# Kernel optimization log

Measured on AMD Instinct MI355X. Metric: run time of the kernel, lower is better.

Reference implementation:

```python
import jax, jax.numpy as jnp
import numpy as np

POOL = 3            # pool_size for this detection level
CENTER_TOP_NUM = 100
CENTER_THRES = 0.1
INST_THRES = 0.4


def _pool2d(x, op, k):
    """Stride-1 SAME pooling on NCHW, matching torch pad=(k-1)//2.
    avg matches torch avg_pool2d default count_include_pad=True (divide by k*k)."""
    if op == 'max':
        return jax.lax.reduce_window(x, -jnp.inf, jax.lax.max,
                                     (1, 1, k, k), (1, 1, 1, 1), 'SAME')
    s = jax.lax.reduce_window(x, 0.0, jax.lax.add,
                              (1, 1, k, k), (1, 1, 1, 1), 'SAME')
    return s / (k * k)


def setup_inputs() -> dict:
    key = jax.random.key(0)
    k1, k2, k3 = jax.random.split(key, 3)
    return {
        'thing_map':    jax.random.normal(k1, (1, 80, 128, 256), jnp.float32),
        'kernel_space': jax.random.normal(k2, (1, 256, 128, 256), jnp.float32),
        'embeddings':   jax.random.normal(k3, (1, 256, 256, 512), jnp.float32),
    }


def reference(thing_map, kernel_space, embeddings):
    B, C, H, W = thing_map.shape
    # --- peak detection (CenterNet-style) ---
    centers = jax.nn.sigmoid(thing_map)
    centers = (centers + _pool2d(centers, 'avg', POOL)) * 0.5
    fmap_max = _pool2d(centers, 'max', 3)
    peak_mask = (fmap_max == centers).astype(centers.dtype)
    centers = centers * peak_mask
    # --- topk over (class, h, w) ---
    K = min(H * W, CENTER_TOP_NUM // 2)  # 50
    flat = centers.reshape(B, C * H * W)
    scores, idx = jax.lax.top_k(flat, K)          # [B, K], sorted descending
    cats = idx // (H * W)                          # [B, K] class ids
    spatial = idx % (H * W)                        # [B, K] spatial index
    # masked_select(score > thres) replaced by a static-shape validity mask
    valid = (scores > CENTER_THRES).astype(scores.dtype)
    # --- sample kernels at peak locations ---
    D = kernel_space.shape[1]
    kflat = kernel_space.reshape(B, D, H * W)      # batch dims (h w)
    kernels = jnp.take_along_axis(kflat, spatial[:, None, :], axis=2)  # [B, D, K]
    kernels = kernels.transpose(0, 2, 1)           # [B, K, D]
    # --- maskifier: dynamic conv of kernels over embeddings, then sigmoid ---
    thing_masks = jax.nn.sigmoid(
        jnp.einsum('bkd,bdhw->bkhw', kernels, embeddings))  # [B, K, He, We]
    # --- mask-based score rescoring ---
    binm = (thing_masks > INST_THRES).astype(thing_masks.dtype)
    score_factor = (thing_masks * binm).sum((-2, -1))
    score_factor = score_factor / jnp.maximum(binm.sum((-2, -1)), 1e-8)
    scores = scores * score_factor * valid
    return thing_masks, scores, cats
```

## Files before the change

### kernel.cpp

```cpp
#include <hip/hip_runtime.h>
#include <hip/hip_bf16.h>
#include <math.h>


constexpr int C   = 80;
constexpr int H   = 128;
constexpr int W   = 256;
constexpr int HW  = H * W;
constexpr int CHW = C * HW;
constexpr int D   = 256;
constexpr int NPIX = 256 * 512;
constexpr int K   = 50;
constexpr int KP  = 52;
constexpr int NBINS = 4096;
constexpr int NREP  = 16;
constexpr int MAXCAND = 8192;
constexpr int SEL_CAP = 4096;
constexpr int MASK_ELEMS = K * NPIX;

constexpr int NBLK  = C * 128;
constexpr int SLOTS = 64;
constexpr int CAP   = NBLK * SLOTS;

constexpr int OFF_PKVAL  = 0;
constexpr int OFF_PKIDX  = CAP;
constexpr int OFF_PKCNT  = 2 * CAP;
constexpr int OFF_HIST   = OFF_PKCNT + NBLK;
constexpr int OFF_CUTBIN = OFF_HIST + NREP * NBINS;
constexpr int OFF_CCOUNT = OFF_CUTBIN + 1;
constexpr int OFF_FNUM   = OFF_CCOUNT + 1;
constexpr int OFF_FDEN   = OFF_FNUM + K;
constexpr int OFF_CVAL   = OFF_FDEN + K;
constexpr int OFF_CIDX   = OFF_CVAL + MAXCAND;
constexpr int OFF_TSCORE = OFF_CIDX + MAXCAND;
constexpr int OFF_TSPAT  = OFF_TSCORE + K;
constexpr int OFF_TCAT   = OFF_TSPAT + K;
constexpr int OFF_A      = (OFF_TCAT + K + 3) & ~3;
constexpr int ZERO_WORDS = NREP * NBINS + 2 + 2 * K;

#define REP13(X) X(0) X(1) X(2) X(3) X(4) X(5) X(6) X(7) X(8) X(9) X(10) X(11) X(12)

__device__ __forceinline__ float sigmoidf(float x) {
    return 1.0f / (1.0f + expf(-x));
}

__device__ __forceinline__ int value_bin(float v) {
    int b = (int)(v * (float)NBINS);
    return b > NBINS - 1 ? NBINS - 1 : b;
}

constexpr int TW = 64, TH = 4;
constexpr int SW = TW + 4, SH = TH + 4;
constexpr int CW = TW + 2, CH2 = TH + 2;

__global__ __launch_bounds__(256) void peaks_kernel(
        const float* __restrict__ x, float* __restrict__ ws) {
    __shared__ float ssig[SH][SW];
    __shared__ float scen[CH2][CW];
    __shared__ int   wcnt[4];

    const int tid = threadIdx.x;
    const int b  = blockIdx.x;
    const int c  = b >> 7;
    const int t  = b & 127;
    const int h0 = (t >> 2) * TH;
    const int w0 = (t & 3) * TW;
    const float* xc = x + c * HW;

    for (int l = tid; l < SH * SW; l += 256) {
        int r = l / SW, q = l - r * SW;
        int h = h0 + r - 2, w = w0 + q - 2;
        float s = 0.0f;
        if ((unsigned)h < (unsigned)H && (unsigned)w < (unsigned)W)
            s = sigmoidf(xc[(h << 8) + w]);
        ssig[r][q] = s;
    }
    __syncthreads();

    for (int l = tid; l < CH2 * CW; l += 256) {
        int r = l / CW, q = l - r * CW;
        int h = h0 + r - 1, w = w0 + q - 1;
        float cv = -INFINITY;
        if ((unsigned)h < (unsigned)H && (unsigned)w < (unsigned)W) {
            float s0 = ssig[r + 1][q + 1];
            float sum = 0.0f;
            #pragma unroll
            for (int dh = 0; dh < 3; dh++)
                #pragma unroll
                for (int dw = 0; dw < 3; dw++)
                    sum += ssig[r + dh][q + dw];
            cv = 0.5f * (s0 + sum / 9.0f);
        }
        scen[r][q] = cv;
    }
    __syncthreads();

    const int dw = tid & 63, dh = tid >> 6;
    float c0 = scen[dh + 1][dw + 1];
    float m = c0;
    #pragma unroll
    for (int i = 0; i < 3; i++)
        #pragma unroll
        for (int j = 0; j < 3; j++)
            m = fmaxf(m, scen[dh + i][dw + j]);
    const bool peak = (c0 == m);
    const int idx = c * HW + ((h0 + dh) << 8) + (w0 + dw);

    if (peak) {
        atomicAdd((int*)ws + OFF_HIST + (b & (NREP - 1)) * NBINS + value_bin(c0), 1);
    }

    unsigned long long mk = __ballot(peak);
    const int lane = tid & 63, wv = tid >> 6;
    if (lane == 0) wcnt[wv] = __popcll(mk);
    __syncthreads();
    int woff = 0;
    #pragma unroll
    for (int i = 0; i < 4; i++) if (i < wv) woff += wcnt[i];
    if (peak) {
        int rank = woff + __popcll(mk & ((1ull << lane) - 1ull));
        if (rank < SLOTS) {
            ws[OFF_PKVAL + b * SLOTS + rank] = c0;
            ((int*)ws)[OFF_PKIDX + b * SLOTS + rank] = idx;
        }
    }
    if (tid == 0) {
        int total = wcnt[0] + wcnt[1] + wcnt[2] + wcnt[3];
        ((int*)ws)[OFF_PKCNT + b] = total > SLOTS ? SLOTS : total;
    }
}

__global__ void scan_kernel(float* ws) {
    __shared__ int shist[NBINS];
    __shared__ int chunk[256];
    const int* hist = (const int*)ws + OFF_HIST;
    int t = threadIdx.x;
    for (int b = t; b < NBINS; b += 256) {
        int s = 0;
        #pragma unroll
        for (int r = 0; r < NREP; r++) s += hist[r * NBINS + b];
        shist[b] = s;
    }
    __syncthreads();
    int s = 0;
    #pragma unroll
    for (int b = t * 16; b < t * 16 + 16; b++) s += shist[b];
    chunk[t] = s;
    __syncthreads();
    if (t == 0) {
        int cum = 0, cutbin = 0;
        bool found = false;
        for (int ch = 255; ch >= 0 && !found; ch--) {
            if (cum + chunk[ch] >= K) {
                for (int b = ch * 16 + 15; b >= ch * 16; b--) {
                    cum += shist[b];
                    if (cum >= K) { cutbin = b; found = true; break; }
                }
            } else {
                cum += chunk[ch];
            }
        }
        ((int*)ws)[OFF_CUTBIN] = found ? cutbin : 0;
    }
}

__global__ void gather_kernel(float* ws) {
    int q = blockIdx.x * 256 + threadIdx.x;
    int bid = q >> 6;
    int i = q & 63;
    int cnt = ((const int*)ws)[OFF_PKCNT + bid];
    if (i < cnt) {
        float v = ws[OFF_PKVAL + q];
        int cutbin = ((const int*)ws)[OFF_CUTBIN];
        if (value_bin(v) >= cutbin) {
            int pos = atomicAdd((int*)ws + OFF_CCOUNT, 1);
            if (pos < MAXCAND) {
                ws[OFF_CVAL + pos] = v;
                ((int*)ws)[OFF_CIDX + pos] = ((const int*)ws)[OFF_PKIDX + q];
            }
        }
    }
}

__global__ void select_kernel(float* ws) {
    __shared__ float sv[SEL_CAP];
    __shared__ int   si[SEL_CAP];
    __shared__ unsigned smask[MAXCAND / 32];
    const float* cval = ws + OFF_CVAL;
    const int*   cidx = (const int*)ws + OFF_CIDX;
    int n = ((const int*)ws)[OFF_CCOUNT];
    if (n > MAXCAND) n = MAXCAND;
    int t = threadIdx.x;

    int cap = n < SEL_CAP ? n : SEL_CAP;
    for (int q = t; q < cap; q += 64) { sv[q] = cval[q]; si[q] = cidx[q]; }
    for (int q = t; q < MAXCAND / 32; q += 64) smask[q] = 0u;
    __syncthreads();

    for (int j = 0; j < K; j++) {
        float bv = -1e30f; int bi = 0x7fffffff; int bp = -1;
        for (int q = t; q < n; q += 64) {
            if (smask[q >> 5] & (1u << (q & 31))) continue;
            float v; int id;
            if (q < SEL_CAP) { v = sv[q]; id = si[q]; }
            else             { v = cval[q]; id = cidx[q]; }
            if (v > bv || (v == bv && id < bi)) { bv = v; bi = id; bp = q; }
        }
        #pragma unroll
        for (int m = 1; m < 64; m <<= 1) {
            float ov = __shfl_xor(bv, m);
            int   oi = __shfl_xor(bi, m);
            int   op = __shfl_xor(bp, m);
            if (ov > bv || (ov == bv && oi < bi)) { bv = ov; bi = oi; bp = op; }
        }
        if (t == 0) {
            float score = (bp >= 0) ? bv : 0.0f;
            int   idx   = (bp >= 0) ? bi : 0;
            ws[OFF_TSCORE + j] = score;
            ((int*)ws)[OFF_TSPAT + j] = idx & (HW - 1);
            ((int*)ws)[OFF_TCAT + j]  = idx >> 15;
            if (bp >= 0) smask[bp >> 5] |= (1u << (bp & 31));
        }
        __syncthreads();
    }
}

__global__ void gatherA_kernel(const float* __restrict__ ksp, float* __restrict__ ws) {
    int k = blockIdx.x;
    int d = threadIdx.x;
    float v = 0.0f;
    if (k < K) {
        int sp = ((const int*)ws)[OFF_TSPAT + k];
        v = ksp[d * HW + sp];
    }
    ws[OFF_A + d * KP + k] = v;
}

#define FMAROW(i) { const float4 a_ = Arow[i]; \
    c##i.x = fmaf(e, a_.x, c##i.x); \
    c##i.y = fmaf(e, a_.y, c##i.y); \
    c##i.z = fmaf(e, a_.z, c##i.z); \
    c##i.w = fmaf(e, a_.w, c##i.w); }

__global__ __launch_bounds__(256) void gemm_kernel(
        const float* __restrict__ emb,
        const float* __restrict__ At,
        float* __restrict__ out) {
    const int n = blockIdx.x * 256 + threadIdx.x;
    const float4* __restrict__ Af = (const float4*)At;

#define DECLC(i) float4 c##i = make_float4(0.0f, 0.0f, 0.0f, 0.0f);
    REP13(DECLC)
#undef DECLC

    const float* __restrict__ ep = emb + n;
    float cur0 = ep[(size_t)0 * NPIX];
    float cur1 = ep[(size_t)1 * NPIX];
    float cur2 = ep[(size_t)2 * NPIX];
    float cur3 = ep[(size_t)3 * NPIX];

    for (int d = 0; d < D - 4; d += 4) {
        const float* q = ep + (size_t)(d + 4) * NPIX;
        float nxt0 = q[0];
        float nxt1 = q[(size_t)1 * NPIX];
        float nxt2 = q[(size_t)2 * NPIX];
        float nxt3 = q[(size_t)3 * NPIX];
        { const float4* Arow = Af + (d + 0) * 13; const float e = cur0; REP13(FMAROW) }
        { const float4* Arow = Af + (d + 1) * 13; const float e = cur1; REP13(FMAROW) }
        { const float4* Arow = Af + (d + 2) * 13; const float e = cur2; REP13(FMAROW) }
        { const float4* Arow = Af + (d + 3) * 13; const float e = cur3; REP13(FMAROW) }
        cur0 = nxt0; cur1 = nxt1; cur2 = nxt2; cur3 = nxt3;
    }
    { const float4* Arow = Af + (D - 4) * 13; const float e = cur0; REP13(FMAROW) }
    { const float4* Arow = Af + (D - 3) * 13; const float e = cur1; REP13(FMAROW) }
    { const float4* Arow = Af + (D - 2) * 13; const float e = cur2; REP13(FMAROW) }
    { const float4* Arow = Af + (D - 1) * 13; const float e = cur3; REP13(FMAROW) }

    float* op = out + n;
#define EPI(i) \
    if (4*(i)+0 < K) op[(size_t)(4*(i)+0) * NPIX] = 1.0f/(1.0f+expf(-c##i.x)); \
    if (4*(i)+1 < K) op[(size_t)(4*(i)+1) * NPIX] = 1.0f/(1.0f+expf(-c##i.y)); \
    if (4*(i)+2 < K) op[(size_t)(4*(i)+2) * NPIX] = 1.0f/(1.0f+expf(-c##i.z)); \
    if (4*(i)+3 < K) op[(size_t)(4*(i)+3) * NPIX] = 1.0f/(1.0f+expf(-c##i.w));
    REP13(EPI)
#undef EPI
}

__global__ __launch_bounds__(256) void rescore_kernel(
        const float* __restrict__ masks,
        float* __restrict__ fnum,
        float* __restrict__ fden) {
    const int k = blockIdx.x;
    const float4* mk = (const float4*)(masks + (size_t)k * NPIX);
    float a = 0.0f; float b = 0.0f;
    int base = blockIdx.y * 2048 + threadIdx.x;
    #pragma unroll
    for (int r = 0; r < 8; r++) {
        float4 v = mk[base + r * 256];
        if (v.x > 0.4f) { a += v.x; b += 1.0f; }
        if (v.y > 0.4f) { a += v.y; b += 1.0f; }
        if (v.z > 0.4f) { a += v.z; b += 1.0f; }
        if (v.w > 0.4f) { a += v.w; b += 1.0f; }
    }
    a += __shfl_xor(a, 1);  b += __shfl_xor(b, 1);
    a += __shfl_xor(a, 2);  b += __shfl_xor(b, 2);
    a += __shfl_xor(a, 4);  b += __shfl_xor(b, 4);
    a += __shfl_xor(a, 8);  b += __shfl_xor(b, 8);
    a += __shfl_xor(a, 16); b += __shfl_xor(b, 16);
    a += __shfl_xor(a, 32); b += __shfl_xor(b, 32);
    __shared__ float sa[4], sb[4];
    int wave = threadIdx.x >> 6;
    if ((threadIdx.x & 63) == 0) { sa[wave] = a; sb[wave] = b; }
    __syncthreads();
    if (threadIdx.x == 0) {
        atomicAdd(&fnum[k], sa[0] + sa[1] + sa[2] + sa[3]);
        atomicAdd(&fden[k], sb[0] + sb[1] + sb[2] + sb[3]);
    }
}

__global__ void finalize_kernel(const float* __restrict__ ws, float* __restrict__ out) {
    int j = threadIdx.x;
    if (j < K) {
        float s = ws[OFF_TSCORE + j];
        float num = ws[OFF_FNUM + j];
        float den = ws[OFF_FDEN + j];
        float factor = num / fmaxf(den, 1e-8f);
        float valid = (s > 0.1f) ? 1.0f : 0.0f;
        out[MASK_ELEMS + j]     = s * factor * valid;
        out[MASK_ELEMS + K + j] = (float)(((const int*)ws)[OFF_TCAT + j]);
    }
}

extern "C" void kernel_launch(void* const* d_in, const int* in_sizes, int n_in,
                              void* d_out, int out_size, void* d_ws, size_t ws_size,
                              hipStream_t stream) {
    const float* thing_map = (const float*)d_in[0];
    const float* ksp       = (const float*)d_in[1];
    const float* emb       = (const float*)d_in[2];
    float* out = (float*)d_out;
    float* ws  = (float*)d_ws;

    hipMemsetAsync(ws + OFF_HIST, 0, (size_t)ZERO_WORDS * 4, stream);

    peaks_kernel<<<NBLK, 256, 0, stream>>>(thing_map, ws);
    scan_kernel<<<1, 256, 0, stream>>>(ws);
    gather_kernel<<<CAP / 256, 256, 0, stream>>>(ws);
    select_kernel<<<1, 64, 0, stream>>>(ws);
    gatherA_kernel<<<KP, D, 0, stream>>>(ksp, ws);
    gemm_kernel<<<NPIX / 256, 256, 0, stream>>>(emb, ws + OFF_A, out);
    rescore_kernel<<<dim3(K, 16), 256, 0, stream>>>(out, ws + OFF_FNUM, ws + OFF_FDEN);
    finalize_kernel<<<1, 64, 0, stream>>>(ws, out);
}
```

Before: 376.8 us.

## Split GEMM reduction dimension across two half-blocks with shared-memory combine

Each block now covers 128 pixels, with the two halves of its 256 threads each summing over half of the D=256 reduction dimension. The partial sums are then combined through shared memory before the sigmoid epilogue. This doubles the grid size for more parallelism and latency hiding, and deepens the embedding prefetch to two groups of four loads. In exchange it adds a shared-memory round trip, a block barrier, and half the threads sitting idle during the store epilogue.

```diff
diff --git a/kernel.cpp b/kernel.cpp
--- a/kernel.cpp
+++ b/kernel.cpp
@@ -246,44 +246,69 @@
         const float* __restrict__ emb,
         const float* __restrict__ At,
         float* __restrict__ out) {
-    const int n = blockIdx.x * 256 + threadIdx.x;
-    const float4* __restrict__ Af = (const float4*)At;
+    __shared__ float sP[KP * 128];
+    const int tid = threadIdx.x;
+    const int pxl = tid & 127;
+    const int dh  = tid >> 7;
+    const int n   = blockIdx.x * 128 + pxl;
+    const float4* __restrict__ Af = (const float4*)At + dh * 128 * 13;
 
 #define DECLC(i) float4 c##i = make_float4(0.0f, 0.0f, 0.0f, 0.0f);
     REP13(DECLC)
 #undef DECLC
 
-    const float* __restrict__ ep = emb + n;
-    float cur0 = ep[(size_t)0 * NPIX];
-    float cur1 = ep[(size_t)1 * NPIX];
-    float cur2 = ep[(size_t)2 * NPIX];
-    float cur3 = ep[(size_t)3 * NPIX];
-
-    for (int d = 0; d < D - 4; d += 4) {
-        const float* q = ep + (size_t)(d + 4) * NPIX;
-        float nxt0 = q[0];
-        float nxt1 = q[(size_t)1 * NPIX];
-        float nxt2 = q[(size_t)2 * NPIX];
-        float nxt3 = q[(size_t)3 * NPIX];
-        { const float4* Arow = Af + (d + 0) * 13; const float e = cur0; REP13(FMAROW) }
-        { const float4* Arow = Af + (d + 1) * 13; const float e = cur1; REP13(FMAROW) }
-        { const float4* Arow = Af + (d + 2) * 13; const float e = cur2; REP13(FMAROW) }
-        { const float4* Arow = Af + (d + 3) * 13; const float e = cur3; REP13(FMAROW) }
-        cur0 = nxt0; cur1 = nxt1; cur2 = nxt2; cur3 = nxt3;
-    }
-    { const float4* Arow = Af + (D - 4) * 13; const float e = cur0; REP13(FMAROW) }
-    { const float4* Arow = Af + (D - 3) * 13; const float e = cur1; REP13(FMAROW) }
-    { const float4* Arow = Af + (D - 2) * 13; const float e = cur2; REP13(FMAROW) }
-    { const float4* Arow = Af + (D - 1) * 13; const float e = cur3; REP13(FMAROW) }
-
-    float* op = out + n;
-#define EPI(i) \
-    if (4*(i)+0 < K) op[(size_t)(4*(i)+0) * NPIX] = 1.0f/(1.0f+expf(-c##i.x)); \
-    if (4*(i)+1 < K) op[(size_t)(4*(i)+1) * NPIX] = 1.0f/(1.0f+expf(-c##i.y)); \
-    if (4*(i)+2 < K) op[(size_t)(4*(i)+2) * NPIX] = 1.0f/(1.0f+expf(-c##i.z)); \
-    if (4*(i)+3 < K) op[(size_t)(4*(i)+3) * NPIX] = 1.0f/(1.0f+expf(-c##i.w));
-    REP13(EPI)
+    const float* __restrict__ ep = emb + (size_t)dh * 128 * NPIX + n;
+    float e0 = ep[(size_t)0 * NPIX], e1 = ep[(size_t)1 * NPIX];
+    float e2 = ep[(size_t)2 * NPIX], e3 = ep[(size_t)3 * NPIX];
+    float f0 = ep[(size_t)4 * NPIX], f1 = ep[(size_t)5 * NPIX];
+    float f2 = ep[(size_t)6 * NPIX], f3 = ep[(size_t)7 * NPIX];
+
+    for (int d = 0; d < 120; d += 4) {
+        const float* q = ep + (size_t)(d + 8) * NPIX;
+        float g0 = q[0];
+        float g1 = q[(size_t)1 * NPIX];
+        float g2 = q[(size_t)2 * NPIX];
+        float g3 = q[(size_t)3 * NPIX];
+        { const float4* Arow = Af + (d + 0) * 13; const float e = e0; REP13(FMAROW) }
+        { const float4* Arow = Af + (d + 1) * 13; const float e = e1; REP13(FMAROW) }
+        { const float4* Arow = Af + (d + 2) * 13; const float e = e2; REP13(FMAROW) }
+        { const float4* Arow = Af + (d + 3) * 13; const float e = e3; REP13(FMAROW) }
+        e0 = f0; e1 = f1; e2 = f2; e3 = f3;
+        f0 = g0; f1 = g1; f2 = g2; f3 = g3;
+    }
+    { const float4* Arow = Af + 120 * 13; const float e = e0; REP13(FMAROW) }
+    { const float4* Arow = Af + 121 * 13; const float e = e1; REP13(FMAROW) }
+    { const float4* Arow = Af + 122 * 13; const float e = e2; REP13(FMAROW) }
+    { const float4* Arow = Af + 123 * 13; const float e = e3; REP13(FMAROW) }
+    { const float4* Arow = Af + 124 * 13; const float e = f0; REP13(FMAROW) }
+    { const float4* Arow = Af + 125 * 13; const float e = f1; REP13(FMAROW) }
+    { const float4* Arow = Af + 126 * 13; const float e = f2; REP13(FMAROW) }
+    { const float4* Arow = Af + 127 * 13; const float e = f3; REP13(FMAROW) }
+
+    if (dh == 1) {
+#define WRT(i) \
+        sP[(4*(i)+0)*128 + pxl] = c##i.x; \
+        sP[(4*(i)+1)*128 + pxl] = c##i.y; \
+        sP[(4*(i)+2)*128 + pxl] = c##i.z; \
+        sP[(4*(i)+3)*128 + pxl] = c##i.w;
+        REP13(WRT)
+#undef WRT
+    }
+    __syncthreads();
+    if (dh == 0) {
+        float* op = out + n;
+#define EPI(i) { \
+        float sx = c##i.x + sP[(4*(i)+0)*128 + pxl]; \
+        float sy = c##i.y + sP[(4*(i)+1)*128 + pxl]; \
+        float sz = c##i.z + sP[(4*(i)+2)*128 + pxl]; \
+        float sw = c##i.w + sP[(4*(i)+3)*128 + pxl]; \
+        if (4*(i)+0 < K) op[(size_t)(4*(i)+0) * NPIX] = 1.0f/(1.0f+expf(-sx)); \
+        if (4*(i)+1 < K) op[(size_t)(4*(i)+1) * NPIX] = 1.0f/(1.0f+expf(-sy)); \
+        if (4*(i)+2 < K) op[(size_t)(4*(i)+2) * NPIX] = 1.0f/(1.0f+expf(-sz)); \
+        if (4*(i)+3 < K) op[(size_t)(4*(i)+3) * NPIX] = 1.0f/(1.0f+expf(-sw)); }
+        REP13(EPI)
 #undef EPI
+    }
 }
 
 __global__ __launch_bounds__(256) void rescore_kernel(
@@ -347,7 +372,7 @@
     gather_kernel<<<CAP / 256, 256, 0, stream>>>(ws);
     select_kernel<<<1, 64, 0, stream>>>(ws);
     gatherA_kernel<<<KP, D, 0, stream>>>(ksp, ws);
-    gemm_kernel<<<NPIX / 256, 256, 0, stream>>>(emb, ws + OFF_A, out);
+    gemm_kernel<<<NPIX / 128, 256, 0, stream>>>(emb, ws + OFF_A, out);
     rescore_kernel<<<dim3(K, 16), 256, 0, stream>>>(out, ws + OFF_FNUM, ws + OFF_FDEN);
     finalize_kernel<<<1, 64, 0, stream>>>(ws, out);
 }
```

Result: slower. 551.6 us (+46.4%).
